# Optimization experiments

Measured on AMD Instinct MI355X. Metric: run time of the kernel, lower is better.

## Reference

```python
import jax, jax.numpy as jnp
import numpy as np

CH = 180
HEDS = (2, 4, 6)
WSIZES = (4, 8, 12)
NUM_GLOBAL = 4

def setup_inputs() -> dict:
    key = jax.random.key(0)
    ks = jax.random.split(key, 5)
    b, H, W = 2, 192, 192
    return {
        "x": jax.random.normal(ks[0], (b, CH, H, W), jnp.float32),
        "proj_w": jax.random.normal(ks[1], (2 * CH, CH), jnp.float32) * 0.05,
        "proj_b": jnp.zeros((2 * CH,), jnp.float32),
        "gn_gamma": jnp.ones((2 * CH,), jnp.float32),
        "gn_beta": jnp.zeros((2 * CH,), jnp.float32),
        "token_scores": jax.random.normal(ks[2], (8, 8), jnp.float32) * 0.02,
        "scale_weights": jnp.ones((3,), jnp.float32),
        "fuse_w": jax.random.normal(ks[3], (CH, CH), jnp.float32) * 0.05,
        "fuse_b": jnp.zeros((CH,), jnp.float32),
    }

def _group_norm(x, gamma, beta, groups=2, eps=1e-5):
    b, c, h, w = x.shape
    xg = x.reshape(b, groups, c // groups, h, w)
    mu = xg.mean(axis=(2, 3, 4), keepdims=True)
    var = xg.var(axis=(2, 3, 4), keepdims=True)
    xn = ((xg - mu) / jnp.sqrt(var + eps)).reshape(b, c, h, w)
    return xn * gamma[None, :, None, None] + beta[None, :, None, None]

def _gmmsa(x, proj_w, proj_b, gn_gamma, gn_beta, token_scores, scale_weights, fuse_w, fuse_b):
    b, c, H, W = x.shape
    # project_inp: 1x1 conv -> GroupNorm(2 groups)
    xp = jnp.einsum('oc,bchw->bohw', proj_w, x) + proj_b[None, :, None, None]
    xp = _group_norm(xp, gn_gamma, gn_beta)
    split = 2 * c // 3
    xs = [xp[:, i * split:(i + 1) * split] for i in range(3)]
    # top-k global token indices from row 0 of token_scores (indices in [0,8))
    _, gidx = jax.lax.top_k(token_scores[0], NUM_GLOBAL)  # (4,)
    ys, atns = [], []
    for i in range(3):
        ws = WSIZES[i]
        he = HEDS[i]
        ch = split // (2 * he)  # per-head channels
        # shifts > 0 branch
        x_ = jnp.roll(xs[i], (ws // 2, -ws // 2), axis=(2, 3))
        nh, nw = H // ws, W // ws
        # 'b (qv c he) (h dh) (w dw) -> qv (b h w) he (dh dw) c'
        t = x_.reshape(b, 2, ch, he, nh, ws, nw, ws)
        t = t.transpose(1, 0, 4, 6, 3, 5, 7, 2)  # qv,b,nh,nw,he,dh,dw,c
        t = t.reshape(2, b * nh * nw, he, ws * ws, ch)
        q, v = t[0], t[1]
        q_l = q * (he ** -0.5)  # note: scaled by num-heads, as in the source
        # local windowed attention: q_l @ q_l^T (k is transpose of scaled q)
        attn = jax.nn.softmax(jnp.einsum('whtc,whsc->whts', q_l, q_l), axis=-1)
        out_local = jnp.einsum('whts,whsc->whtc', attn, v)
        # global-token recompute + scatter
        q_g = q_l[:, :, gidx, :]
        attn_g = jax.nn.softmax(jnp.einsum('whtc,whsc->whts', q_g, q_l), axis=-1)
        out_attn = attn.at[:, :, gidx, :].set(attn_g)
        out_g = jnp.einsum('whts,whsc->whtc', attn_g, v)
        out_win = out_local.at[:, :, gidx, :].set(out_g)
        # '(b h w) he (dh dw) c -> b (c he) (h dh) (w dw)'
        y_ = out_win.reshape(b, nh, nw, he, ws, ws, ch)
        y_ = y_.transpose(0, 6, 3, 1, 4, 2, 5).reshape(b, ch * he, H, W)
        y_ = jnp.roll(y_, (-ws // 2, ws // 2), axis=(2, 3))
        ys.append(y_)
        atns.append(out_attn)
    # AFFM fusion: scale each branch, concat on channels, 1x1 conv
    y_fused = jnp.concatenate([scale_weights[i] * ys[i] for i in range(3)], axis=1)
    y = jnp.einsum('oc,bchw->bohw', fuse_w, y_fused) + fuse_b[None, :, None, None]
    return y, atns

def reference(x, proj_w, proj_b, gn_gamma, gn_beta, token_scores, scale_weights, fuse_w, fuse_b):
    y, atns = _gmmsa(x, proj_w, proj_b, gn_gamma, gn_beta, token_scores, scale_weights, fuse_w, fuse_b)
    return (y, atns[0], atns[1], atns[2])
```

## Files before the change

kernel.cpp:

```cpp
#include <hip/hip_runtime.h>
#include <hip/hip_bf16.h>
#include <cstdint>


typedef __hip_bfloat16 bf16;
typedef __hip_bfloat162 bf162;
typedef __attribute__((ext_vector_type(8))) __bf16 bf16x8;
typedef __attribute__((ext_vector_type(4))) float f32x4;

#define IMG 192
#define PIX (IMG*IMG)
#define CIN 180
#define CMID 360

__device__ __forceinline__ float b2f(bf16 v){ return __bfloat162float(v); }
__device__ __forceinline__ bf16 f2b(float v){ return __float2bfloat16(v); }

__device__ __forceinline__ void st2(float* p, float a, float b){
    *reinterpret_cast<float2*>(p) = make_float2(a, b);
}

__device__ __forceinline__ void split2(float x, unsigned short& h, unsigned short& l){
    __bf16 bh = (__bf16)x;
    float fh = (float)bh;
    __bf16 bl = (__bf16)(x - fh);
    h = __builtin_bit_cast(unsigned short, bh);
    l = __builtin_bit_cast(unsigned short, bl);
}

union FragU { unsigned short s[8]; uint32_t u[4]; bf16x8 v; };

__device__ __forceinline__ f32x4 mf(bf16x8 a, bf16x8 b, f32x4 c){
    return __builtin_amdgcn_mfma_f32_16x16x32_bf16(a, b, c, 0, 0, 0);
}

__global__ void k_prep(const float* __restrict__ pw, const float* __restrict__ fw,
                       bf16* __restrict__ WFp, bf16* __restrict__ WFf)
{
    const int which = blockIdx.y;
    const int MI = which ? 12 : 24;
    const int M  = which ? 180 : 360;
    const float* W = which ? fw : pw;
    bf16* out = which ? WFf : WFp;
    int gid = blockIdx.x*256 + threadIdx.x;
    if (gid >= MI*6*64) return;
    const int l  = gid & 63;
    const int s  = (gid >> 6) % 6;
    const int mm = gid / (6*64);
    const int am = l & 15, kg = l >> 4;
    const int row = mm*16 + am;
    FragU h, lo;
#pragma unroll
    for (int j=0;j<8;j++){
        int k = s*32 + kg*8 + j;
        float x = (row < M && k < 180) ? W[(size_t)row*180 + k] : 0.f;
        unsigned short hh, ll;
        split2(x, hh, ll);
        h.s[j] = hh; lo.s[j] = ll;
    }
    size_t base = (size_t)gid*8;
    *reinterpret_cast<bf16x8*>(out + base) = h.v;
    *reinterpret_cast<bf16x8*>(out + (size_t)MI*6*64*8 + base) = lo.v;
}

template<int MT, int MI, int MPW, bool XF32, bool STATS, typename XT, typename YT>
__global__ __launch_bounds__(256, 2) void k_gemm_mfma(
    const bf16* __restrict__ WF, const float* __restrict__ Bv,
    const XT* __restrict__ X, YT* __restrict__ Y, float* __restrict__ stats)
{
    constexpr int LX = 66;
    constexpr int NWORDS = XF32 ? 192*LX : 96*LX;
    __shared__ uint32_t lds[NWORDS];
    __shared__ float red[4][4];

    const int tid = threadIdx.x;
    const int bz  = blockIdx.z;
    const int p0  = blockIdx.x * 64;
    const int w  = tid >> 6, l = tid & 63;
    const int mw = w >> 1,  nw = w & 1;
    const int am = l & 15,  kg = l >> 4;

    if constexpr (XF32) {
        for (int idx = tid; idx < 192*32; idx += 256){
            int k = idx >> 5, p2 = idx & 31;
            float2 v = make_float2(0.f, 0.f);
            if (k < 180)
                v = *reinterpret_cast<const float2*>(X + ((size_t)(bz*180 + k))*PIX + p0 + 2*p2);
            *reinterpret_cast<float2*>(&lds[k*LX + 2*p2]) = v;
        }
    } else {
        const unsigned short* Xu = reinterpret_cast<const unsigned short*>(X);
        for (int idx = tid; idx < 96*32; idx += 256){
            int k2 = idx >> 5, p2 = idx & 31;
            uint32_t d0 = 0, d1 = 0;
            if (2*k2 < 180){
                uint32_t a = *reinterpret_cast<const uint32_t*>(Xu + ((size_t)(bz*180 + 2*k2  ))*PIX + p0 + 2*p2);
                uint32_t b = *reinterpret_cast<const uint32_t*>(Xu + ((size_t)(bz*180 + 2*k2+1))*PIX + p0 + 2*p2);
                d0 = (a & 0xFFFFu) | (b << 16);
                d1 = (a >> 16)     | (b & 0xFFFF0000u);
            }
            lds[k2*LX + 2*p2]     = d0;
            lds[k2*LX + 2*p2 + 1] = d1;
        }
    }
    __syncthreads();

    bf16x8 Bh[6][2], Bl[6][2];
#pragma unroll
    for (int s=0;s<6;s++){
#pragma unroll
        for (int j=0;j<2;j++){
            const int col = (nw*2 + j)*16 + am;
            FragU h;
            if constexpr (XF32) {
                FragU lo;
                const float* lf = reinterpret_cast<const float*>(lds);
#pragma unroll
                for (int j2=0;j2<4;j2++){
                    int k0 = s*32 + kg*8 + 2*j2;
                    float f0 = lf[(k0  )*LX + col];
                    float f1 = lf[(k0+1)*LX + col];
                    unsigned short h0,l0,h1,l1;
                    split2(f0,h0,l0); split2(f1,h1,l1);
                    h.u[j2]  = (uint32_t)h0 | ((uint32_t)h1 << 16);
                    lo.u[j2] = (uint32_t)l0 | ((uint32_t)l1 << 16);
                }
                Bh[s][j] = h.v; Bl[s][j] = lo.v;
            } else {
#pragma unroll
                for (int j2=0;j2<4;j2++)
                    h.u[j2] = lds[(s*16 + kg*4 + j2)*LX + col];
                Bh[s][j] = h.v;
            }
        }
    }
    __syncthreads();

    float* scr = reinterpret_cast<float*>(lds) + w*(16*36);
    float s0=0.f,s1=0.f,q0=0.f,q1=0.f;

    for (int i=0;i<MPW;i++){
        const int mm = mw*MPW + i;
        bf16x8 Ah[6], Al[6];
#pragma unroll
        for (int s=0;s<6;s++){
            Ah[s] = *reinterpret_cast<const bf16x8*>(WF + (((size_t)(0*MI + mm)*6 + s)*64 + l)*8);
            Al[s] = *reinterpret_cast<const bf16x8*>(WF + (((size_t)(1*MI + mm)*6 + s)*64 + l)*8);
        }
        f32x4 aA[2], aB[2];
#pragma unroll
        for (int j=0;j<2;j++){ aA[j]=(f32x4){0,0,0,0}; aB[j]=(f32x4){0,0,0,0}; }
#pragma unroll
        for (int s=0;s<6;s++){
#pragma unroll
            for (int j=0;j<2;j++){
                f32x4 t = (s&1) ? aB[j] : aA[j];
                t = mf(Ah[s], Bh[s][j], t);
                if constexpr (XF32) {
                    t = mf(Ah[s], Bl[s][j], t);
                    t = mf(Al[s], Bh[s][j], t);
                } else {
                    t = mf(Al[s], Bh[s][j], t);
                }
                if (s&1) aB[j]=t; else aA[j]=t;
            }
        }
#pragma unroll
        for (int j=0;j<2;j++){
#pragma unroll
            for (int r=0;r<4;r++)
                scr[(kg*4+r)*36 + j*16 + am] = aA[j][r] + aB[j][r];
        }
        asm volatile("s_waitcnt lgkmcnt(0)" ::: "memory");
        const int row = l >> 2, c8 = (l & 3)*8;
        float4 fa = *reinterpret_cast<const float4*>(&scr[row*36 + c8]);
        float4 fb = *reinterpret_cast<const float4*>(&scr[row*36 + c8 + 4]);
        const int o = mm*16 + row;
        if (o < MT){
            const float bb = Bv[o];
            float v[8] = {fa.x+bb, fa.y+bb, fa.z+bb, fa.w+bb,
                          fb.x+bb, fb.y+bb, fb.z+bb, fb.w+bb};
            if (STATS){
                float ls=0.f, lq=0.f;
#pragma unroll
                for (int j=0;j<8;j++){ ls += v[j]; lq = fmaf(v[j], v[j], lq); }
                if (o < 180){ s0 += ls; q0 += lq; } else { s1 += ls; q1 += lq; }
            }
            size_t yi = ((size_t)bz*MT + o)*PIX + p0 + nw*32 + c8;
            if constexpr (sizeof(YT)==2){
                unsigned short u[8];
#pragma unroll
                for (int j=0;j<8;j++) u[j] = __builtin_bit_cast(unsigned short, f2b(v[j]));
                *reinterpret_cast<uint4*>(&Y[yi]) = *reinterpret_cast<uint4*>(u);
            } else {
                *reinterpret_cast<float4*>(&Y[yi])   = make_float4(v[0],v[1],v[2],v[3]);
                *reinterpret_cast<float4*>(&Y[yi+4]) = make_float4(v[4],v[5],v[6],v[7]);
            }
        }
        asm volatile("s_waitcnt lgkmcnt(0)" ::: "memory");
    }

    if (STATS){
#pragma unroll
        for (int off=32; off>0; off>>=1){
            s0 += __shfl_down(s0, off); s1 += __shfl_down(s1, off);
            q0 += __shfl_down(q0, off); q1 += __shfl_down(q1, off);
        }
        if (l==0){ red[0][w]=s0; red[1][w]=s1; red[2][w]=q0; red[3][w]=q1; }
        __syncthreads();
        if (tid==0){
            float r0=red[0][0]+red[0][1]+red[0][2]+red[0][3];
            float r1=red[1][0]+red[1][1]+red[1][2]+red[1][3];
            float r2=red[2][0]+red[2][1]+red[2][2]+red[2][3];
            float r3=red[3][0]+red[3][1]+red[3][2]+red[3][3];
            atomicAdd(&stats[(bz*2+0)*2+0], r0);
            atomicAdd(&stats[(bz*2+1)*2+0], r1);
            atomicAdd(&stats[(bz*2+0)*2+1], r2);
            atomicAdd(&stats[(bz*2+1)*2+1], r3);
        }
    }
}

__global__ void k_stats(float* stats)
{
    int i = threadIdx.x;
    if (i < 4) {
        const float n = 180.0f*36864.0f;
        float mu  = stats[i*2] / n;
        float var = stats[i*2+1]/n - mu*mu;
        stats[8 + i*2]     = mu;
        stats[8 + i*2 + 1] = rsqrtf(var + 1e-5f);
    }
}

template<int WS, int HE, int CHN, int SI, int SPLIT, int RROW, int NSC>
__global__ __launch_bounds__(256) void k_attn(
    const bf16* __restrict__ xp, const float* __restrict__ musig,
    const float* __restrict__ gamma, const float* __restrict__ beta,
    const float* __restrict__ swt,
    float* __restrict__ atn, bf16* __restrict__ yf)
{
    constexpr int T = WS*WS;
    constexpr int NWIN = IMG/WS;
    constexpr int TR = T/SPLIT;
    constexpr int PP = TR/RROW;
    constexpr int SLEN = T/NSC;
    constexpr int ST = TR + 1;
    constexpr int TP = T + 1;
    __shared__ float qs[CHN*TP];
    __shared__ float vs[CHN*TP];
    __shared__ float Sm[T*ST];
    __shared__ float rinv[TR];

    const int tid = threadIdx.x;
    const int wid = blockIdx.x;
    const int head = blockIdx.y;
    const int tb = blockIdx.z * TR;
    const int bi = wid / (NWIN*NWIN);
    const int r2 = wid - bi*(NWIN*NWIN);
    const int wy = r2 / NWIN;
    const int wx = r2 - wy*NWIN;

    for (int idx = tid; idx < 2*T*CHN; idx += 256) {
        int qv = idx / (T*CHN);
        int rem = idx - qv*(T*CHN);
        int c = rem / T;
        int t = rem - c*T;
        int chan = SI*120 + qv*60 + c*HE + head;
        int r = t / WS, cc = t - r*WS;
        int sh = wy*WS + r - WS/2;  if (sh < 0) sh += IMG;
        int sw = wx*WS + cc + WS/2; if (sw >= IMG) sw -= IMG;
        float val = b2f(xp[((size_t)(bi*CMID + chan)*IMG + sh)*IMG + sw]);
        int g = (chan >= 180) ? 1 : 0;
        float mu = musig[(bi*2+g)*2+0];
        float rs = musig[(bi*2+g)*2+1];
        float xn = fmaf((val - mu)*rs, gamma[chan], beta[chan]);
        if (qv) vs[c*TP+t] = xn; else qs[c*TP+t] = xn;
    }
    __syncthreads();

    constexpr float invHE = 1.0f/(float)HE;
    for (int item = tid; item < PP*NSC; item += 256) {
        int sc = item / PP;
        int p2 = item - sc*PP;
        int tl0 = p2*RROW;
        float qreg[RROW][CHN];
#pragma unroll
        for (int rr=0; rr<RROW; ++rr)
#pragma unroll
            for (int c=0;c<CHN;c++)
                qreg[rr][c] = qs[c*TP + tb + tl0 + rr];
        for (int j=0;j<SLEN;++j) {
            int s = sc*SLEN + j;
            float d[RROW];
#pragma unroll
            for (int rr=0;rr<RROW;++rr) d[rr]=0.f;
#pragma unroll
            for (int c=0;c<CHN;c++){
                float qc = qs[c*TP + s];
#pragma unroll
                for (int rr=0;rr<RROW;++rr)
                    d[rr] = fmaf(qreg[rr][c], qc, d[rr]);
            }
#pragma unroll
            for (int rr=0;rr<RROW;++rr)
                Sm[s*ST + tl0 + rr] = d[rr]*invHE;
        }
    }
    __syncthreads();

    for (int tl = tid; tl < TR; tl += 256) {
        float mx = -1e30f;
        for (int s=0;s<T;s++) mx = fmaxf(mx, Sm[s*ST + tl]);
        float sum = 0.f;
        for (int s=0;s<T;s++){
            float e = __expf(Sm[s*ST + tl] - mx);
            Sm[s*ST + tl] = e;
            sum += e;
        }
        rinv[tl] = 1.0f/sum;
    }
    __syncthreads();

    {
        size_t abase = ((size_t)wid*HE + head)*(size_t)(T*T) + (size_t)tb*T;
        for (int e2 = tid; e2 < TR*T/2; e2 += 256) {
            int e = e2*2;
            int tl = e / T;
            int s = e - tl*T;
            float ri = rinv[tl];
            st2(atn + abase + e, Sm[s*ST + tl]*ri, Sm[(s+1)*ST + tl]*ri);
        }
    }

    float swf = swt[SI];
    for (int item = tid; item < CHN*(TR/2); item += 256) {
        int c = item / (TR/2);
        int tp = item - c*(TR/2);
        int tl0 = tp*2;
        float a0=0.f, a1=0.f;
        for (int s=0;s<T;s++){
            float vv = vs[c*TP + s];
            a0 = fmaf(Sm[s*ST + tl0],   vv, a0);
            a1 = fmaf(Sm[s*ST + tl0+1], vv, a1);
        }
        int yc = SI*60 + c*HE + head;
#pragma unroll
        for (int k2=0;k2<2;k2++){
            int tl = tl0 + k2;
            int t = tb + tl;
            float ov = (k2 ? a1 : a0) * rinv[tl] * swf;
            int r = t / WS, cc = t - r*WS;
            int sh = wy*WS + r - WS/2;  if (sh < 0) sh += IMG;
            int sw = wx*WS + cc + WS/2; if (sw >= IMG) sw -= IMG;
            yf[((size_t)(bi*CIN + yc)*IMG + sh)*IMG + sw] = f2b(ov);
        }
    }
}

extern "C" void kernel_launch(void* const* d_in, const int* in_sizes, int n_in,
                              void* d_out, int out_size, void* d_ws, size_t ws_size,
                              hipStream_t stream)
{
    (void)in_sizes; (void)n_in; (void)out_size; (void)ws_size;
    const float* x   = (const float*)d_in[0];
    const float* pw  = (const float*)d_in[1];
    const float* pb  = (const float*)d_in[2];
    const float* gg  = (const float*)d_in[3];
    const float* gb  = (const float*)d_in[4];
    const float* swt = (const float*)d_in[6];
    const float* fw  = (const float*)d_in[7];
    const float* fb  = (const float*)d_in[8];

    float* out  = (float*)d_out;
    float* atn0 = out + 13271040;
    float* atn1 = out + 15630336;
    float* atn2 = out + 34504704;

    char* ws = (char*)d_ws;
    bf16*  xp    = (bf16*)ws;
    bf16*  yf    = (bf16*)(ws + 53084160);
    float* stats = (float*)(ws + 79626240);
    bf16*  WFp   = (bf16*)(ws + 79626304);
    bf16*  WFf   = (bf16*)(ws + 79921216);

    hipMemsetAsync(stats, 0, 64, stream);
    k_prep<<<dim3(36,2,1), 256, 0, stream>>>(pw, fw, WFp, WFf);
    k_gemm_mfma<360,24,12,true,true,float,bf16><<<dim3(576,1,2), 256, 0, stream>>>(WFp, pb, x, xp, stats);
    k_stats<<<1, 64, 0, stream>>>(stats);
    k_attn<4, 2, 30, 0, 1, 1, 16><<<dim3(4608,2,1), 256, 0, stream>>>(xp, stats+8, gg, gb, swt, atn0, yf);
    k_attn<8, 4, 15, 1, 1, 2, 8 ><<<dim3(1152,4,1), 256, 0, stream>>>(xp, stats+8, gg, gb, swt, atn1, yf);
    k_attn<12,6, 10, 2, 2, 2, 8 ><<<dim3(512, 6,2), 256, 0, stream>>>(xp, stats+8, gg, gb, swt, atn2, yf);
    k_gemm_mfma<180,12,6,false,false,bf16,float><<<dim3(576,1,2), 256, 0, stream>>>(WFf, fb, yf, out, nullptr);
}
```

Baseline: 957.3 us.

## Pre-split GEMM input into bf16 hi/lo in LDS, direct epilogue, fused attention halves

The projection GEMM now splits fp32 inputs into bf16 hi/lo once while staging into LDS, so fragment loads are plain word reads. The epilogue that staged results through an LDS scratch buffer is removed, and each lane now stores its accumulator elements straight to global memory, giving narrower, less coalesced stores. The attention kernel loads packed bf16 pairs as 32-bit words, runs the softmax with two threads per row combined by a shuffle, and handles both query halves of the 12x12 window in one block. That avoids loading q/v twice at the cost of a serial loop inside the block.

```diff
diff --git a/kernel.cpp b/kernel.cpp
--- a/kernel.cpp
+++ b/kernel.cpp
@@ -63,14 +63,13 @@
     *reinterpret_cast<bf16x8*>(out + (size_t)MI*6*64*8 + base) = lo.v;
 }
 
-template<int MT, int MI, int MPW, bool XF32, bool STATS, typename XT, typename YT>
+template<int MT, int MI, int MPW, int XSPLIT, bool STATS, typename XT, typename YT>
 __global__ __launch_bounds__(256, 2) void k_gemm_mfma(
     const bf16* __restrict__ WF, const float* __restrict__ Bv,
     const XT* __restrict__ X, YT* __restrict__ Y, float* __restrict__ stats)
 {
     constexpr int LX = 66;
-    constexpr int NWORDS = XF32 ? 192*LX : 96*LX;
-    __shared__ uint32_t lds[NWORDS];
+    __shared__ uint32_t lds[XSPLIT*96*LX];
     __shared__ float red[4][4];
 
     const int tid = threadIdx.x;
@@ -80,13 +79,25 @@
     const int mw = w >> 1,  nw = w & 1;
     const int am = l & 15,  kg = l >> 4;
 
-    if constexpr (XF32) {
-        for (int idx = tid; idx < 192*32; idx += 256){
-            int k = idx >> 5, p2 = idx & 31;
-            float2 v = make_float2(0.f, 0.f);
-            if (k < 180)
-                v = *reinterpret_cast<const float2*>(X + ((size_t)(bz*180 + k))*PIX + p0 + 2*p2);
-            *reinterpret_cast<float2*>(&lds[k*LX + 2*p2]) = v;
+    if constexpr (XSPLIT == 2) {
+        for (int idx = tid; idx < 96*32; idx += 256){
+            int k2 = idx >> 5, p2 = idx & 31;
+            uint32_t h0=0,h1=0,lo0=0,lo1=0;
+            if (2*k2 < 180){
+                float2 a = *reinterpret_cast<const float2*>(X + ((size_t)(bz*180 + 2*k2  ))*PIX + p0 + 2*p2);
+                float2 b = *reinterpret_cast<const float2*>(X + ((size_t)(bz*180 + 2*k2+1))*PIX + p0 + 2*p2);
+                unsigned short ha,la,hb,lb;
+                split2(a.x,ha,la); split2(b.x,hb,lb);
+                h0  = (uint32_t)ha | ((uint32_t)hb << 16);
+                lo0 = (uint32_t)la | ((uint32_t)lb << 16);
+                split2(a.y,ha,la); split2(b.y,hb,lb);
+                h1  = (uint32_t)ha | ((uint32_t)hb << 16);
+                lo1 = (uint32_t)la | ((uint32_t)lb << 16);
+            }
+            lds[k2*LX + 2*p2]           = h0;
+            lds[k2*LX + 2*p2 + 1]       = h1;
+            lds[96*LX + k2*LX + 2*p2]   = lo0;
+            lds[96*LX + k2*LX + 2*p2+1] = lo1;
         }
     } else {
         const unsigned short* Xu = reinterpret_cast<const unsigned short*>(X);
@@ -112,31 +123,20 @@
         for (int j=0;j<2;j++){
             const int col = (nw*2 + j)*16 + am;
             FragU h;
-            if constexpr (XF32) {
+#pragma unroll
+            for (int j2=0;j2<4;j2++)
+                h.u[j2] = lds[(s*16 + kg*4 + j2)*LX + col];
+            Bh[s][j] = h.v;
+            if constexpr (XSPLIT == 2) {
                 FragU lo;
-                const float* lf = reinterpret_cast<const float*>(lds);
-#pragma unroll
-                for (int j2=0;j2<4;j2++){
-                    int k0 = s*32 + kg*8 + 2*j2;
-                    float f0 = lf[(k0  )*LX + col];
-                    float f1 = lf[(k0+1)*LX + col];
-                    unsigned short h0,l0,h1,l1;
-                    split2(f0,h0,l0); split2(f1,h1,l1);
-                    h.u[j2]  = (uint32_t)h0 | ((uint32_t)h1 << 16);
-                    lo.u[j2] = (uint32_t)l0 | ((uint32_t)l1 << 16);
-                }
-                Bh[s][j] = h.v; Bl[s][j] = lo.v;
-            } else {
 #pragma unroll
                 for (int j2=0;j2<4;j2++)
-                    h.u[j2] = lds[(s*16 + kg*4 + j2)*LX + col];
-                Bh[s][j] = h.v;
-            }
-        }
-    }
-    __syncthreads();
-
-    float* scr = reinterpret_cast<float*>(lds) + w*(16*36);
+                    lo.u[j2] = lds[96*LX + (s*16 + kg*4 + j2)*LX + col];
+                Bl[s][j] = lo.v;
+            }
+        }
+    }
+
     float s0=0.f,s1=0.f,q0=0.f,q1=0.f;
 
     for (int i=0;i<MPW;i++){
@@ -156,7 +156,7 @@
             for (int j=0;j<2;j++){
                 f32x4 t = (s&1) ? aB[j] : aA[j];
                 t = mf(Ah[s], Bh[s][j], t);
-                if constexpr (XF32) {
+                if constexpr (XSPLIT == 2) {
                     t = mf(Ah[s], Bl[s][j], t);
                     t = mf(Al[s], Bh[s][j], t);
                 } else {
@@ -165,39 +165,24 @@
                 if (s&1) aB[j]=t; else aA[j]=t;
             }
         }
-#pragma unroll
-        for (int j=0;j<2;j++){
-#pragma unroll
-            for (int r=0;r<4;r++)
-                scr[(kg*4+r)*36 + j*16 + am] = aA[j][r] + aB[j][r];
-        }
-        asm volatile("s_waitcnt lgkmcnt(0)" ::: "memory");
-        const int row = l >> 2, c8 = (l & 3)*8;
-        float4 fa = *reinterpret_cast<const float4*>(&scr[row*36 + c8]);
-        float4 fb = *reinterpret_cast<const float4*>(&scr[row*36 + c8 + 4]);
-        const int o = mm*16 + row;
-        if (o < MT){
-            const float bb = Bv[o];
-            float v[8] = {fa.x+bb, fa.y+bb, fa.z+bb, fa.w+bb,
-                          fb.x+bb, fb.y+bb, fb.z+bb, fb.w+bb};
-            if (STATS){
-                float ls=0.f, lq=0.f;
-#pragma unroll
-                for (int j=0;j<8;j++){ ls += v[j]; lq = fmaf(v[j], v[j], lq); }
-                if (o < 180){ s0 += ls; q0 += lq; } else { s1 += ls; q1 += lq; }
-            }
-            size_t yi = ((size_t)bz*MT + o)*PIX + p0 + nw*32 + c8;
-            if constexpr (sizeof(YT)==2){
-                unsigned short u[8];
-#pragma unroll
-                for (int j=0;j<8;j++) u[j] = __builtin_bit_cast(unsigned short, f2b(v[j]));
-                *reinterpret_cast<uint4*>(&Y[yi]) = *reinterpret_cast<uint4*>(u);
-            } else {
-                *reinterpret_cast<float4*>(&Y[yi])   = make_float4(v[0],v[1],v[2],v[3]);
-                *reinterpret_cast<float4*>(&Y[yi+4]) = make_float4(v[4],v[5],v[6],v[7]);
-            }
-        }
-        asm volatile("s_waitcnt lgkmcnt(0)" ::: "memory");
+        const int orow0 = mm*16 + kg*4;
+#pragma unroll
+        for (int r=0;r<4;r++){
+            const int o = orow0 + r;
+            if (o < MT){
+                const float bb = Bv[o];
+#pragma unroll
+                for (int j=0;j<2;j++){
+                    float v = aA[j][r] + aB[j][r] + bb;
+                    size_t yi = ((size_t)bz*MT + o)*PIX + p0 + (nw*2+j)*16 + am;
+                    if constexpr (sizeof(YT)==2) Y[yi] = f2b(v); else Y[yi] = v;
+                    if (STATS){
+                        if (o < 180){ s0 += v; q0 = fmaf(v,v,q0); }
+                        else        { s1 += v; q1 = fmaf(v,v,q1); }
+                    }
+                }
+            }
+        }
     }
 
     if (STATS){
@@ -233,7 +218,7 @@
     }
 }
 
-template<int WS, int HE, int CHN, int SI, int SPLIT, int RROW, int NSC>
+template<int WS, int HE, int CHN, int SI, int HALVES, int RROW, int NSC>
 __global__ __launch_bounds__(256) void k_attn(
     const bf16* __restrict__ xp, const float* __restrict__ musig,
     const float* __restrict__ gamma, const float* __restrict__ beta,
@@ -242,11 +227,12 @@
 {
     constexpr int T = WS*WS;
     constexpr int NWIN = IMG/WS;
-    constexpr int TR = T/SPLIT;
+    constexpr int TR = T/HALVES;
     constexpr int PP = TR/RROW;
     constexpr int SLEN = T/NSC;
     constexpr int ST = TR + 1;
     constexpr int TP = T + 1;
+    constexpr int SEG = WS/2;
     __shared__ float qs[CHN*TP];
     __shared__ float vs[CHN*TP];
     __shared__ float Sm[T*ST];
@@ -255,106 +241,124 @@
     const int tid = threadIdx.x;
     const int wid = blockIdx.x;
     const int head = blockIdx.y;
-    const int tb = blockIdx.z * TR;
     const int bi = wid / (NWIN*NWIN);
     const int r2 = wid - bi*(NWIN*NWIN);
     const int wy = r2 / NWIN;
     const int wx = r2 - wy*NWIN;
 
-    for (int idx = tid; idx < 2*T*CHN; idx += 256) {
-        int qv = idx / (T*CHN);
-        int rem = idx - qv*(T*CHN);
-        int c = rem / T;
-        int t = rem - c*T;
+    const uint32_t* xpu = reinterpret_cast<const uint32_t*>(xp);
+    for (int it = tid; it < 2*CHN*WS*SEG; it += 256) {
+        int seg  = it % SEG;
+        int tmp  = it / SEG;
+        int r    = tmp % WS;
+        int tmp2 = tmp / WS;
+        int c    = tmp2 % CHN;
+        int qv   = tmp2 / CHN;
         int chan = SI*120 + qv*60 + c*HE + head;
-        int r = t / WS, cc = t - r*WS;
-        int sh = wy*WS + r - WS/2;  if (sh < 0) sh += IMG;
-        int sw = wx*WS + cc + WS/2; if (sw >= IMG) sw -= IMG;
-        float val = b2f(xp[((size_t)(bi*CMID + chan)*IMG + sh)*IMG + sw]);
+        int sh = wy*WS + r - WS/2;      if (sh < 0)    sh += IMG;
+        int sw0 = wx*WS + 2*seg + WS/2; if (sw0 >= IMG) sw0 -= IMG;
+        uint32_t d = xpu[((size_t)(bi*CMID + chan)*IMG + sh)*(IMG/2) + (sw0>>1)];
+        float f0 = __uint_as_float(d << 16);
+        float f1 = __uint_as_float(d & 0xffff0000u);
         int g = (chan >= 180) ? 1 : 0;
         float mu = musig[(bi*2+g)*2+0];
         float rs = musig[(bi*2+g)*2+1];
-        float xn = fmaf((val - mu)*rs, gamma[chan], beta[chan]);
-        if (qv) vs[c*TP+t] = xn; else qs[c*TP+t] = xn;
+        float ga = gamma[chan], be = beta[chan];
+        float x0 = fmaf((f0 - mu)*rs, ga, be);
+        float x1 = fmaf((f1 - mu)*rs, ga, be);
+        int t = r*WS + 2*seg;
+        float* dst = qv ? vs : qs;
+        dst[c*TP + t]     = x0;
+        dst[c*TP + t + 1] = x1;
     }
     __syncthreads();
 
     constexpr float invHE = 1.0f/(float)HE;
-    for (int item = tid; item < PP*NSC; item += 256) {
-        int sc = item / PP;
-        int p2 = item - sc*PP;
-        int tl0 = p2*RROW;
-        float qreg[RROW][CHN];
-#pragma unroll
-        for (int rr=0; rr<RROW; ++rr)
-#pragma unroll
-            for (int c=0;c<CHN;c++)
-                qreg[rr][c] = qs[c*TP + tb + tl0 + rr];
-        for (int j=0;j<SLEN;++j) {
-            int s = sc*SLEN + j;
-            float d[RROW];
-#pragma unroll
-            for (int rr=0;rr<RROW;++rr) d[rr]=0.f;
-#pragma unroll
-            for (int c=0;c<CHN;c++){
-                float qc = qs[c*TP + s];
+    const float swf = swt[SI];
+
+    for (int ph = 0; ph < HALVES; ++ph) {
+        const int tb = ph*TR;
+
+        for (int item = tid; item < PP*NSC; item += 256) {
+            int sc = item / PP;
+            int p2 = item - sc*PP;
+            int tl0 = p2*RROW;
+            float qreg[RROW][CHN];
+#pragma unroll
+            for (int rr=0; rr<RROW; ++rr)
+#pragma unroll
+                for (int c=0;c<CHN;c++)
+                    qreg[rr][c] = qs[c*TP + tb + tl0 + rr];
+            for (int j=0;j<SLEN;++j) {
+                int s = sc*SLEN + j;
+                float d[RROW];
+#pragma unroll
+                for (int rr=0;rr<RROW;++rr) d[rr]=0.f;
+#pragma unroll
+                for (int c=0;c<CHN;c++){
+                    float qc = qs[c*TP + s];
+#pragma unroll
+                    for (int rr=0;rr<RROW;++rr)
+                        d[rr] = fmaf(qreg[rr][c], qc, d[rr]);
+                }
 #pragma unroll
                 for (int rr=0;rr<RROW;++rr)
-                    d[rr] = fmaf(qreg[rr][c], qc, d[rr]);
-            }
-#pragma unroll
-            for (int rr=0;rr<RROW;++rr)
-                Sm[s*ST + tl0 + rr] = d[rr]*invHE;
-        }
-    }
-    __syncthreads();
-
-    for (int tl = tid; tl < TR; tl += 256) {
-        float mx = -1e30f;
-        for (int s=0;s<T;s++) mx = fmaxf(mx, Sm[s*ST + tl]);
-        float sum = 0.f;
-        for (int s=0;s<T;s++){
-            float e = __expf(Sm[s*ST + tl] - mx);
-            Sm[s*ST + tl] = e;
-            sum += e;
-        }
-        rinv[tl] = 1.0f/sum;
-    }
-    __syncthreads();
-
-    {
-        size_t abase = ((size_t)wid*HE + head)*(size_t)(T*T) + (size_t)tb*T;
-        for (int e2 = tid; e2 < TR*T/2; e2 += 256) {
-            int e = e2*2;
-            int tl = e / T;
-            int s = e - tl*T;
-            float ri = rinv[tl];
-            st2(atn + abase + e, Sm[s*ST + tl]*ri, Sm[(s+1)*ST + tl]*ri);
-        }
-    }
-
-    float swf = swt[SI];
-    for (int item = tid; item < CHN*(TR/2); item += 256) {
-        int c = item / (TR/2);
-        int tp = item - c*(TR/2);
-        int tl0 = tp*2;
-        float a0=0.f, a1=0.f;
-        for (int s=0;s<T;s++){
-            float vv = vs[c*TP + s];
-            a0 = fmaf(Sm[s*ST + tl0],   vv, a0);
-            a1 = fmaf(Sm[s*ST + tl0+1], vv, a1);
-        }
-        int yc = SI*60 + c*HE + head;
-#pragma unroll
-        for (int k2=0;k2<2;k2++){
-            int tl = tl0 + k2;
-            int t = tb + tl;
-            float ov = (k2 ? a1 : a0) * rinv[tl] * swf;
-            int r = t / WS, cc = t - r*WS;
-            int sh = wy*WS + r - WS/2;  if (sh < 0) sh += IMG;
-            int sw = wx*WS + cc + WS/2; if (sw >= IMG) sw -= IMG;
-            yf[((size_t)(bi*CIN + yc)*IMG + sh)*IMG + sw] = f2b(ov);
-        }
+                    Sm[s*ST + tl0 + rr] = d[rr]*invHE;
+            }
+        }
+        __syncthreads();
+
+        for (int pr = tid; pr < 2*TR; pr += 256) {
+            int tl = pr >> 1, hf = pr & 1;
+            int sBeg = hf*(T/2);
+            float mx = -1e30f;
+            for (int s=sBeg; s<sBeg+T/2; ++s) mx = fmaxf(mx, Sm[s*ST + tl]);
+            mx = fmaxf(mx, __shfl_xor(mx, 1));
+            float sum = 0.f;
+            for (int s=sBeg; s<sBeg+T/2; ++s){
+                float e = __expf(Sm[s*ST + tl] - mx);
+                Sm[s*ST + tl] = e;
+                sum += e;
+            }
+            sum += __shfl_xor(sum, 1);
+            if (!hf) rinv[tl] = 1.0f/sum;
+        }
+        __syncthreads();
+
+        {
+            size_t abase = ((size_t)wid*HE + head)*(size_t)(T*T) + (size_t)tb*T;
+            for (int e2 = tid; e2 < TR*T/2; e2 += 256) {
+                int e = e2*2;
+                int tl = e / T;
+                int s = e - tl*T;
+                float ri = rinv[tl];
+                st2(atn + abase + e, Sm[s*ST + tl]*ri, Sm[(s+1)*ST + tl]*ri);
+            }
+        }
+
+        for (int item = tid; item < CHN*(TR/2); item += 256) {
+            int c = item / (TR/2);
+            int tp = item - c*(TR/2);
+            int tl0 = tp*2;
+            float a0=0.f, a1=0.f;
+            for (int s=0;s<T;s++){
+                float vv = vs[c*TP + s];
+                a0 = fmaf(Sm[s*ST + tl0],   vv, a0);
+                a1 = fmaf(Sm[s*ST + tl0+1], vv, a1);
+            }
+            int yc = SI*60 + c*HE + head;
+#pragma unroll
+            for (int k2=0;k2<2;k2++){
+                int tl = tl0 + k2;
+                int t = tb + tl;
+                float ov = (k2 ? a1 : a0) * rinv[tl] * swf;
+                int r = t / WS, cc = t - r*WS;
+                int sh = wy*WS + r - WS/2;  if (sh < 0) sh += IMG;
+                int sw = wx*WS + cc + WS/2; if (sw >= IMG) sw -= IMG;
+                yf[((size_t)(bi*CIN + yc)*IMG + sh)*IMG + sw] = f2b(ov);
+            }
+        }
+        if (HALVES > 1) __syncthreads();
     }
 }
 
@@ -386,10 +390,10 @@
 
     hipMemsetAsync(stats, 0, 64, stream);
     k_prep<<<dim3(36,2,1), 256, 0, stream>>>(pw, fw, WFp, WFf);
-    k_gemm_mfma<360,24,12,true,true,float,bf16><<<dim3(576,1,2), 256, 0, stream>>>(WFp, pb, x, xp, stats);
+    k_gemm_mfma<360,24,12,2,true,float,bf16><<<dim3(576,1,2), 256, 0, stream>>>(WFp, pb, x, xp, stats);
     k_stats<<<1, 64, 0, stream>>>(stats);
     k_attn<4, 2, 30, 0, 1, 1, 16><<<dim3(4608,2,1), 256, 0, stream>>>(xp, stats+8, gg, gb, swt, atn0, yf);
     k_attn<8, 4, 15, 1, 1, 2, 8 ><<<dim3(1152,4,1), 256, 0, stream>>>(xp, stats+8, gg, gb, swt, atn1, yf);
-    k_attn<12,6, 10, 2, 2, 2, 8 ><<<dim3(512, 6,2), 256, 0, stream>>>(xp, stats+8, gg, gb, swt, atn2, yf);
-    k_gemm_mfma<180,12,6,false,false,bf16,float><<<dim3(576,1,2), 256, 0, stream>>>(WFf, fb, yf, out, nullptr);
-}
+    k_attn<12,6, 10, 2, 2, 2, 8 ><<<dim3(512, 6,1), 256, 0, stream>>>(xp, stats+8, gg, gb, swt, atn2, yf);
+    k_gemm_mfma<180,12,6,1,false,bf16,float><<<dim3(576,1,2), 256, 0, stream>>>(WFf, fb, yf, out, nullptr);
+}
```

Result: faster. 824.8 us (-13.8%).
